# Kernel optimization log

Hardware: AMD Instinct MI355X
Metric: run time of the kernel (lower is better)

## Reference

```python
import jax, jax.numpy as jnp
import numpy as np

N, G, E, F, H = 100000, 32768, 1000000, 128, 128

def _mlp(x, w1, b1, w2, b2):
    # Linear -> SiLU -> Linear
    return jax.nn.silu(x @ w1 + b1) @ w2 + b2

def setup_inputs() -> dict:
    key = jax.random.key(0)
    ks = jax.random.split(key, 24)
    s = 0.02
    p = lambda k, shp: (jax.random.normal(k, shp, dtype=jnp.float32) * s)
    inp = {
        "node_features": jax.random.normal(ks[0], (N, F), dtype=jnp.float32),
        "node_pos": jax.random.normal(ks[1], (N, 3), dtype=jnp.float32),
        "grid_pos": jax.random.normal(ks[2], (G, 3), dtype=jnp.float32),
        "edge_index": jax.random.randint(ks[3], (2, E), 0, G, dtype=jnp.int64),
        "orientations": jax.random.normal(ks[4], (N, 3, 3), dtype=jnp.float32),
        # node_model
        "nw1": p(ks[5], (F, H)), "nb1": p(ks[6], (H,)),
        "nw2": p(ks[7], (H, H)), "nb2": p(ks[8], (H,)),
        # edge_model
        "ew1": p(ks[9], (6, H)), "eb1": p(ks[10], (H,)),
        "ew2": p(ks[11], (H, H)), "eb2": p(ks[12], (H,)),
        # message_model
        "mw1": p(ks[13], (2 * H, H)), "mb1": p(ks[14], (H,)),
        "mw2": p(ks[15], (H, H)), "mb2": p(ks[16], (H,)),
        # update_model
        "uw1": p(ks[17], (H, H)), "ub1": p(ks[18], (H,)),
        "uw2": p(ks[19], (H, H)), "ub2": p(ks[20], (H,)),
    }
    return inp

def reference(node_features, node_pos, grid_pos, edge_index, orientations,
              nw1, nb1, nw2, nb2, ew1, eb1, ew2, eb2,
              mw1, mb1, mw2, mb2, uw1, ub1, uw2, ub2):
    src, tgt = edge_index[0], edge_index[1]
    # node MLP on all points [N, H]
    node_h = _mlp(node_features, nw1, nb1, nw2, nb2)
    # per-edge geometry
    pos_src = node_pos[src]                     # [E, 3]
    rel_pos = grid_pos[tgt] - pos_src           # [E, 3]
    # bmm(rel_pos[e,1,3], orientations[src][e,3,3]) -> [E, 3]
    rot = jnp.einsum("ej,ejk->ek", rel_pos, orientations[src])
    edge_attr = jnp.concatenate([pos_src, rot], axis=-1)       # [E, 6]
    edge_h = _mlp(edge_attr, ew1, eb1, ew2, eb2)               # [E, H]
    msg_in = jnp.concatenate([node_h[src], edge_h], axis=-1)   # [E, 2H]
    msg = _mlp(msg_in, mw1, mb1, mw2, mb2)                     # [E, H]
    # scatter-mean to grid
    num_grid = grid_pos.shape[0]
    sums = jax.ops.segment_sum(msg, tgt, num_segments=num_grid)             # [G, H]
    counts = jax.ops.segment_sum(jnp.ones((msg.shape[0],), msg.dtype), tgt,
                                 num_segments=num_grid)
    grid_feat = sums / jnp.clip(counts, 1.0)[:, None]
    return _mlp(grid_feat, uw1, ub1, uw2, ub2)
```

## Files before the change

### kernel.cpp

```cpp
#include <hip/hip_runtime.h>

#define P 136

typedef __attribute__((ext_vector_type(8))) short short8;
typedef __attribute__((ext_vector_type(4))) float f32x4;

__device__ __forceinline__ unsigned short f2bf(float f) {
  union { float f; unsigned u; } v; v.f = f;
  unsigned u = v.u + 0x7fffu + ((v.u >> 16) & 1u);
  return (unsigned short)(u >> 16);
}
__device__ __forceinline__ float bf2f(unsigned short h) {
  union { unsigned u; float f; } v; v.u = ((unsigned)h) << 16;
  return v.f;
}
__device__ __forceinline__ unsigned pack2bf(float x, float y) {
  union { float f; unsigned u; } a, b; a.f = x; b.f = y;
  return __builtin_amdgcn_perm(b.u + 0x8000u, a.u + 0x8000u, 0x07060302u);
}
__device__ __forceinline__ float silu_f(float x) {
  float e = __expf(-x);
  return x * __builtin_amdgcn_rcpf(1.0f + e);
}

__device__ __forceinline__ void load_A128(const unsigned short* __restrict__ W,
                                          int m0w, int l16, int q, short8 a[2][4]) {
#pragma unroll
  for (int rt = 0; rt < 2; ++rt)
#pragma unroll
    for (int kt = 0; kt < 4; ++kt)
      a[rt][kt] = *(const short8*)&W[(m0w + rt * 16 + l16) * 128 + kt * 32 + q * 8];
}

template <int CT, bool INIT>
__device__ __forceinline__ void gemm_T(const short8 a[2][4],
                                       const unsigned short* sB,
                                       int l16, int q, f32x4 acc[2][CT]) {
  const f32x4 Z = (f32x4){0.f, 0.f, 0.f, 0.f};
#pragma unroll
  for (int kt = 0; kt < 4; ++kt)
#pragma unroll
    for (int ct = 0; ct < CT; ++ct) {
      short8 b = *(const short8*)&sB[(ct * 16 + l16) * P + kt * 32 + q * 8];
      f32x4 c0 = (INIT && kt == 0) ? Z : acc[0][ct];
      f32x4 c1 = (INIT && kt == 0) ? Z : acc[1][ct];
      acc[0][ct] = __builtin_amdgcn_mfma_f32_16x16x32_bf16(a[0][kt], b, c0, 0, 0, 0);
      acc[1][ct] = __builtin_amdgcn_mfma_f32_16x16x32_bf16(a[1][kt], b, c1, 0, 0, 0);
    }
}

template <bool SILU, int CT>
__device__ __forceinline__ void epilogue_T(const f32x4 acc[2][CT], const float* bias,
                                           unsigned short* sOut, int m0w, int l16,
                                           int q) {
#pragma unroll
  for (int rt = 0; rt < 2; ++rt) {
    int f0 = m0w + rt * 16 + q * 4;
    float4 bv = *(const float4*)&bias[f0];
#pragma unroll
    for (int ct = 0; ct < CT; ++ct) {
      float v0 = acc[rt][ct][0] + bv.x, v1 = acc[rt][ct][1] + bv.y;
      float v2 = acc[rt][ct][2] + bv.z, v3 = acc[rt][ct][3] + bv.w;
      if (SILU) { v0 = silu_f(v0); v1 = silu_f(v1); v2 = silu_f(v2); v3 = silu_f(v3); }
      uint2 w; w.x = pack2bf(v0, v1); w.y = pack2bf(v2, v3);
      *(uint2*)&sOut[(ct * 16 + l16) * P + f0] = w;
    }
  }
}

__global__ __launch_bounds__(256) void fold_hist_kernel(
    const float* __restrict__ nw1, const float* __restrict__ nw2,
    const float* __restrict__ nb2, const float* __restrict__ ew2,
    const float* __restrict__ eb2, const float* __restrict__ mw1,
    const float* __restrict__ mb1, const float* __restrict__ mw2,
    const float* __restrict__ uw1, const float* __restrict__ uw2,
    const float* __restrict__ ew1,
    unsigned short* __restrict__ nw1t, unsigned short* __restrict__ wnt,
    unsigned short* __restrict__ wct, unsigned short* __restrict__ mw2t,
    unsigned short* __restrict__ uw1t, unsigned short* __restrict__ uw2t,
    unsigned short* __restrict__ ew1t8,
    float* __restrict__ bn, float* __restrict__ bc,
    const int* __restrict__ eidx, int* __restrict__ hist, int E) {
  if (blockIdx.x >= 64) {
    int e0 = (blockIdx.x - 64) * 2048 + threadIdx.x * 8;
    if (e0 + 7 < E && (E & 3) == 0) {
      int4 t0 = *(const int4*)&eidx[E + e0];
      int4 t1 = *(const int4*)&eidx[E + e0 + 4];
      atomicAdd(&hist[t0.x], 1); atomicAdd(&hist[t0.y], 1);
      atomicAdd(&hist[t0.z], 1); atomicAdd(&hist[t0.w], 1);
      atomicAdd(&hist[t1.x], 1); atomicAdd(&hist[t1.y], 1);
      atomicAdd(&hist[t1.z], 1); atomicAdd(&hist[t1.w], 1);
    } else {
#pragma unroll
      for (int k = 0; k < 8; ++k) {
        int e = e0 + k;
        if (e < E) atomicAdd(&hist[eidx[E + e]], 1);
      }
    }
    return;
  }
  int b = blockIdx.x * 2 + (threadIdx.x >> 7);
  int t = threadIdx.x & 127;
  float accn = 0.f, accc = 0.f;
  for (int j = 0; j < 128; ++j) {
    accn += nw2[t * 128 + j] * mw1[j * 128 + b];
    accc += ew2[t * 128 + j] * mw1[(128 + j) * 128 + b];
  }
  wnt[b * 128 + t] = f2bf(accn);
  wct[b * 128 + t] = f2bf(accc);
  nw1t[b * 128 + t] = f2bf(nw1[t * 128 + b]);
  mw2t[b * 128 + t] = f2bf(mw2[t * 128 + b]);
  uw1t[b * 128 + t] = f2bf(uw1[t * 128 + b]);
  uw2t[b * 128 + t] = f2bf(uw2[t * 128 + b]);
  if (t < 8) ew1t8[b * 8 + t] = (t < 6) ? f2bf(ew1[t * 128 + b]) : (unsigned short)0;
  if (b == 0) {
    float sn = 0.f, sc = 0.f;
    for (int j = 0; j < 128; ++j) {
      sn += nb2[j] * mw1[j * 128 + t];
      sc += eb2[j] * mw1[(128 + j) * 128 + t];
    }
    bn[t] = sn;
    bc[t] = mb1[t] + sc;
  }
}

__global__ __launch_bounds__(1024) void scan_kernel(const int* __restrict__ hist,
                                                    int* __restrict__ cursor, int G) {
  __shared__ int s[1024];
  int tid = threadIdx.x;
  int per = (G + 1023) >> 10;
  int b0 = tid * per;
  bool vec = ((per & 3) == 0) && ((G & 3) == 0) && (b0 + per <= G);
  int sum = 0;
  if (vec) {
    for (int i = 0; i < per; i += 4) {
      int4 h = *(const int4*)&hist[b0 + i];
      sum += h.x + h.y + h.z + h.w;
    }
  } else {
    for (int i = 0; i < per; ++i)
      if (b0 + i < G) sum += hist[b0 + i];
  }
  s[tid] = sum;
  __syncthreads();
  for (int off = 1; off < 1024; off <<= 1) {
    int v = (tid >= off) ? s[tid - off] : 0;
    __syncthreads();
    s[tid] += v;
    __syncthreads();
  }
  int run = s[tid] - sum;
  if (vec) {
    for (int i = 0; i < per; i += 4) {
      int4 h = *(const int4*)&hist[b0 + i];
      int4 c;
      c.x = run;
      c.y = c.x + h.x;
      c.z = c.y + h.y;
      c.w = c.z + h.z;
      *(int4*)&cursor[b0 + i] = c;
      run = c.w + h.w;
    }
  } else {
    for (int i = 0; i < per; ++i)
      if (b0 + i < G) {
        cursor[b0 + i] = run;
        run += hist[b0 + i];
      }
  }
}

__global__ __launch_bounds__(256, 3) void scatter_node_kernel(
    const int* __restrict__ eidx, int* __restrict__ cursor,
    int2* __restrict__ st, int E, int nNode,
    const float* __restrict__ x, const float* __restrict__ nb1,
    const unsigned short* __restrict__ nw1t, const unsigned short* __restrict__ wnt,
    const float* __restrict__ bn, unsigned short* __restrict__ node_pre, int N) {
  __shared__ __align__(16) unsigned short s_x[128 * P];
  __shared__ __align__(16) float s_b1[128];
  __shared__ __align__(16) float s_bn[128];

  if (blockIdx.x >= (unsigned)nNode) {
    int e0 = (blockIdx.x - nNode) * 2048 + threadIdx.x * 8;
    if (e0 + 7 < E && (E & 3) == 0) {
      int4 s0 = *(const int4*)&eidx[e0];
      int4 s1 = *(const int4*)&eidx[e0 + 4];
      int4 t0 = *(const int4*)&eidx[E + e0];
      int4 t1 = *(const int4*)&eidx[E + e0 + 4];
      int p0 = atomicAdd(&cursor[t0.x], 1);
      int p1 = atomicAdd(&cursor[t0.y], 1);
      int p2 = atomicAdd(&cursor[t0.z], 1);
      int p3 = atomicAdd(&cursor[t0.w], 1);
      int p4 = atomicAdd(&cursor[t1.x], 1);
      int p5 = atomicAdd(&cursor[t1.y], 1);
      int p6 = atomicAdd(&cursor[t1.z], 1);
      int p7 = atomicAdd(&cursor[t1.w], 1);
      st[p0] = make_int2(s0.x, t0.x);
      st[p1] = make_int2(s0.y, t0.y);
      st[p2] = make_int2(s0.z, t0.z);
      st[p3] = make_int2(s0.w, t0.w);
      st[p4] = make_int2(s1.x, t1.x);
      st[p5] = make_int2(s1.y, t1.y);
      st[p6] = make_int2(s1.z, t1.z);
      st[p7] = make_int2(s1.w, t1.w);
    } else {
#pragma unroll
      for (int k = 0; k < 8; ++k) {
        int e = e0 + k;
        if (e < E) {
          int tg = eidx[E + e];
          int pos = atomicAdd(&cursor[tg], 1);
          st[pos] = make_int2(eidx[e], tg);
        }
      }
    }
    return;
  }

  int tid = threadIdx.x;
  long base = (long)blockIdx.x * 128;

#pragma unroll
  for (int i = 0; i < 16; ++i) {
    int flat = tid + i * 256;
    int row = flat >> 5;
    int c4 = (flat & 31) << 2;
    float4 v = make_float4(0.f, 0.f, 0.f, 0.f);
    if (base + row < N) v = *(const float4*)&x[(base + row) * 128 + c4];
    uint2 w; w.x = pack2bf(v.x, v.y); w.y = pack2bf(v.z, v.w);
    *(uint2*)&s_x[row * P + c4] = w;
  }
  if (tid < 128) { s_b1[tid] = nb1[tid]; s_bn[tid] = bn[tid]; }
  __syncthreads();

  int wave = tid >> 6, lane = tid & 63;
  int q = lane >> 4, l16 = lane & 15;
  int m0w = wave * 32;

  short8 a1[2][4];
  load_A128(nw1t, m0w, l16, q, a1);
  f32x4 acc[2][8];
  gemm_T<8, true>(a1, s_x, l16, q, acc);
  __syncthreads();
  epilogue_T<true, 8>(acc, s_b1, s_x, m0w, l16, q);
  __syncthreads();

  short8 a2[2][4];
  load_A128(wnt, m0w, l16, q, a2);
  gemm_T<8, true>(a2, s_x, l16, q, acc);

#pragma unroll
  for (int rt = 0; rt < 2; ++rt) {
    int f0 = m0w + rt * 16 + q * 4;
    float4 bv = *(const float4*)&s_bn[f0];
#pragma unroll
    for (int ct = 0; ct < 8; ++ct) {
      long n = base + ct * 16 + l16;
      if (n < N) {
        uint2 w;
        w.x = pack2bf(acc[rt][ct][0] + bv.x, acc[rt][ct][1] + bv.y);
        w.y = pack2bf(acc[rt][ct][2] + bv.z, acc[rt][ct][3] + bv.w);
        *(uint2*)&node_pre[n * 128 + f0] = w;
      }
    }
  }
}

__global__ __launch_bounds__(256, 3) void edge_kernel(
    const int2* __restrict__ st_sorted, const float* __restrict__ node_pos,
    const float* __restrict__ grid_pos, const float* __restrict__ ori,
    const unsigned short* __restrict__ ew1t8, const float* __restrict__ eb1,
    const unsigned short* __restrict__ wct, const float* __restrict__ bc,
    const unsigned short* __restrict__ node_pre, float* __restrict__ sums, int E) {
  __shared__ __align__(16) unsigned short s_h[128 * P];
  __shared__ int s_src[128];
  __shared__ int s_tgt[128];
  __shared__ __align__(16) float s_eb1[128];
  __shared__ __align__(16) float s_bc[128];

  int tid = threadIdx.x;
  int base = blockIdx.x * 128;

  if (tid < 128) {
    s_eb1[tid] = eb1[tid];
    s_bc[tid] = bc[tid];
    int eg = base + tid;
    int s = 0, tg = -1;
    float a0 = 0.f, a1 = 0.f, a2 = 0.f, a3 = 0.f, a4 = 0.f, a5 = 0.f;
    if (eg < E) {
      int2 st = st_sorted[eg];
      s = st.x; tg = st.y;
      float2 p01 = *(const float2*)&node_pos[s * 3];
      float pz = node_pos[s * 3 + 2];
      float2 g01 = *(const float2*)&grid_pos[tg * 3];
      float gz = grid_pos[tg * 3 + 2];
      float4 o0 = *(const float4*)&ori[(long)s * 9];
      float4 o1 = *(const float4*)&ori[(long)s * 9 + 4];
      float o8 = ori[(long)s * 9 + 8];
      float rx = g01.x - p01.x, ry = g01.y - p01.y, rz = gz - pz;
      a0 = p01.x; a1 = p01.y; a2 = pz;
      a3 = rx * o0.x + ry * o0.w + rz * o1.z;
      a4 = rx * o0.y + ry * o1.x + rz * o1.w;
      a5 = rx * o0.z + ry * o1.y + rz * o8;
    }
    s_src[tid] = s;
    s_tgt[tid] = tg;
    uint4 w0;
    w0.x = pack2bf(a0, a1); w0.y = pack2bf(a2, a3); w0.z = pack2bf(a4, a5); w0.w = 0u;
    *(uint4*)&s_h[tid * P] = w0;
  }

  int wave = tid >> 6, lane = tid & 63;
  int q = lane >> 4, l16 = lane & 15;
  int m0w = wave * 32;
  short8 z8 = (short8){0, 0, 0, 0, 0, 0, 0, 0};
  const f32x4 Z = (f32x4){0.f, 0.f, 0.f, 0.f};

  short8 ae0 = z8, ae1 = z8;
  if (q == 0) {
    ae0 = *(const short8*)&ew1t8[(m0w + l16) * 8];
    ae1 = *(const short8*)&ew1t8[(m0w + 16 + l16) * 8];
  }

  __syncthreads();

  short8 pre[8];
#pragma unroll
  for (int ct = 0; ct < 8; ++ct) {
    long srow = (long)s_src[ct * 16 + l16] * 128;
    pre[ct] = *(const short8*)&node_pre[srow + m0w + q * 8];
  }

  f32x4 acc[2][8];
#pragma unroll
  for (int ct = 0; ct < 8; ++ct) {
    short8 b = z8;
    if (q == 0) b = *(const short8*)&s_h[(ct * 16 + l16) * P];
    acc[0][ct] = __builtin_amdgcn_mfma_f32_16x16x32_bf16(ae0, b, Z, 0, 0, 0);
    acc[1][ct] = __builtin_amdgcn_mfma_f32_16x16x32_bf16(ae1, b, Z, 0, 0, 0);
  }
  __syncthreads();

  epilogue_T<true, 8>(acc, s_eb1, s_h, m0w, l16, q);

  short8 awc[2][4];
  load_A128(wct, m0w, l16, q, awc);

  __syncthreads();

  short8 aI_lo, aI_hi;
#pragma unroll
  for (int j = 0; j < 8; ++j) {
    aI_lo[j] = ((q * 8 + j) == l16) ? (short)0x3F80 : (short)0;
    aI_hi[j] = ((q * 8 + j) == (l16 + 16)) ? (short)0x3F80 : (short)0;
  }
#pragma unroll
  for (int ct = 0; ct < 8; ++ct) {
    acc[0][ct] = __builtin_amdgcn_mfma_f32_16x16x32_bf16(aI_lo, pre[ct], Z, 0, 0, 0);
    acc[1][ct] = __builtin_amdgcn_mfma_f32_16x16x32_bf16(aI_hi, pre[ct], Z, 0, 0, 0);
  }

  gemm_T<8, false>(awc, s_h, l16, q, acc);
  __syncthreads();

  epilogue_T<true, 8>(acc, s_bc, s_h, m0w, l16, q);
  __syncthreads();

  {
    int cp = tid & 63;
    int chunk = tid >> 6;
    int c0 = cp * 2;
    int row0 = chunk * 32;
    float v0 = 0.f, v1 = 0.f;
    int cur = s_tgt[row0];
    for (int r = 0; r < 32; ++r) {
      int row = row0 + r;
      int tg = s_tgt[row];
      if (tg != cur) {
        if (cur >= 0) {
          atomicAdd(&sums[(long)cur * 128 + c0], v0);
          atomicAdd(&sums[(long)cur * 128 + c0 + 1], v1);
        }
        v0 = 0.f; v1 = 0.f; cur = tg;
      }
      unsigned w = *(const unsigned*)&s_h[row * P + c0];
      v0 += bf2f((unsigned short)w);
      v1 += bf2f((unsigned short)(w >> 16));
    }
    if (cur >= 0) {
      atomicAdd(&sums[(long)cur * 128 + c0], v0);
      atomicAdd(&sums[(long)cur * 128 + c0 + 1], v1);
    }
  }
}

__global__ __launch_bounds__(256, 3) void grid_kernel(
    const float* __restrict__ sums, const int* __restrict__ hist,
    const float* __restrict__ mb2, const float* __restrict__ ub1,
    const float* __restrict__ ub2, const unsigned short* __restrict__ mw2t,
    const unsigned short* __restrict__ uw1t, const unsigned short* __restrict__ uw2t,
    float* __restrict__ out, int G) {
  __shared__ __align__(16) unsigned short s_x[32 * P];
  __shared__ __align__(16) float s_bm[128];
  __shared__ __align__(16) float s_b1[128];
  __shared__ __align__(16) float s_b2[128];
  int tid = threadIdx.x;
  long base = (long)blockIdx.x * 32;

#pragma unroll
  for (int i = 0; i < 4; ++i) {
    int flat = tid + i * 256;
    int row = flat >> 5;
    int c4 = (flat & 31) << 2;
    float4 v = make_float4(0.f, 0.f, 0.f, 0.f);
    float inv = 1.f;
    if (base + row < G) {
      v = *(const float4*)&sums[(base + row) * 128 + c4];
      int c = hist[base + row];
      inv = __builtin_amdgcn_rcpf((float)(c < 1 ? 1 : c));
    }
    uint2 w; w.x = pack2bf(v.x * inv, v.y * inv); w.y = pack2bf(v.z * inv, v.w * inv);
    *(uint2*)&s_x[row * P + c4] = w;
  }
  if (tid < 128) { s_bm[tid] = mb2[tid]; s_b1[tid] = ub1[tid]; s_b2[tid] = ub2[tid]; }
  __syncthreads();

  int wave = tid >> 6, lane = tid & 63;
  int q = lane >> 4, l16 = lane & 15;
  int m0w = wave * 32;

  f32x4 acc[2][2];
  short8 aw[2][4];

  load_A128(mw2t, m0w, l16, q, aw);
  gemm_T<2, true>(aw, s_x, l16, q, acc);
  __syncthreads();
  epilogue_T<false, 2>(acc, s_bm, s_x, m0w, l16, q);
  __syncthreads();

  load_A128(uw1t, m0w, l16, q, aw);
  gemm_T<2, true>(aw, s_x, l16, q, acc);
  __syncthreads();
  epilogue_T<true, 2>(acc, s_b1, s_x, m0w, l16, q);
  __syncthreads();

  load_A128(uw2t, m0w, l16, q, aw);
  gemm_T<2, true>(aw, s_x, l16, q, acc);

#pragma unroll
  for (int rt = 0; rt < 2; ++rt) {
    int f0 = m0w + rt * 16 + q * 4;
    float4 bv = *(const float4*)&s_b2[f0];
#pragma unroll
    for (int ct = 0; ct < 2; ++ct) {
      long g = base + ct * 16 + l16;
      if (g < G) {
        float4 o = make_float4(acc[rt][ct][0] + bv.x, acc[rt][ct][1] + bv.y,
                               acc[rt][ct][2] + bv.z, acc[rt][ct][3] + bv.w);
        *(float4*)&out[g * 128 + f0] = o;
      }
    }
  }
}

extern "C" void kernel_launch(void* const* d_in, const int* in_sizes, int n_in,
                              void* d_out, int out_size, void* d_ws, size_t ws_size,
                              hipStream_t stream) {
  const float* x    = (const float*)d_in[0];
  const float* npos = (const float*)d_in[1];
  const float* gpos = (const float*)d_in[2];
  const int*   eidx = (const int*)d_in[3];
  const float* ori  = (const float*)d_in[4];
  const float* nw1 = (const float*)d_in[5];
  const float* nb1 = (const float*)d_in[6];
  const float* nw2 = (const float*)d_in[7];
  const float* nb2 = (const float*)d_in[8];
  const float* ew1 = (const float*)d_in[9];
  const float* eb1 = (const float*)d_in[10];
  const float* ew2 = (const float*)d_in[11];
  const float* eb2 = (const float*)d_in[12];
  const float* mw1 = (const float*)d_in[13];
  const float* mb1 = (const float*)d_in[14];
  const float* mw2 = (const float*)d_in[15];
  const float* mb2 = (const float*)d_in[16];
  const float* uw1 = (const float*)d_in[17];
  const float* ub1 = (const float*)d_in[18];
  const float* uw2 = (const float*)d_in[19];
  const float* ub2 = (const float*)d_in[20];

  int N = in_sizes[0] / 128;
  int G = in_sizes[2] / 3;
  int E = in_sizes[3] / 2;

  char* ws = (char*)d_ws;
  size_t off = 0;
  float* sums = (float*)(ws + off);            off += (size_t)G * 128 * 4;
  int* hist = (int*)(ws + off);                off += (size_t)G * 4;
  int* cursor = (int*)(ws + off);              off += (size_t)G * 4;
  unsigned short* node_pre = (unsigned short*)(ws + off); off += (size_t)N * 128 * 2;
  off = (off + 255) & ~(size_t)255;
  unsigned short* w_nw1t = (unsigned short*)(ws + off); off += 128 * 128 * 2;
  unsigned short* w_wnt  = (unsigned short*)(ws + off); off += 128 * 128 * 2;
  unsigned short* w_wct  = (unsigned short*)(ws + off); off += 128 * 128 * 2;
  unsigned short* w_mw2t = (unsigned short*)(ws + off); off += 128 * 128 * 2;
  unsigned short* w_uw1t = (unsigned short*)(ws + off); off += 128 * 128 * 2;
  unsigned short* w_uw2t = (unsigned short*)(ws + off); off += 128 * 128 * 2;
  unsigned short* w_ew1t8 = (unsigned short*)(ws + off); off += 128 * 8 * 2;
  float* bn = (float*)(ws + off); off += 128 * 4;
  float* bc = (float*)(ws + off); off += 128 * 4;

  int2* st_sorted = (int2*)d_out;

  int nScat = (E + 2047) / 2048;
  int nNode = (N + 127) / 128;
  int nHist = (E + 2047) / 2048;

  hipMemsetAsync(sums, 0, ((size_t)G * 128 + G) * 4, stream);

  fold_hist_kernel<<<64 + nHist, 256, 0, stream>>>(
      nw1, nw2, nb2, ew2, eb2, mw1, mb1, mw2, uw1, uw2, ew1,
      w_nw1t, w_wnt, w_wct, w_mw2t, w_uw1t, w_uw2t, w_ew1t8, bn, bc,
      eidx, hist, E);
  scan_kernel<<<1, 1024, 0, stream>>>(hist, cursor, G);
  scatter_node_kernel<<<nNode + nScat, 256, 0, stream>>>(
      eidx, cursor, st_sorted, E, nNode,
      x, nb1, w_nw1t, w_wnt, bn, node_pre, N);
  edge_kernel<<<(E + 127) / 128, 256, 0, stream>>>(st_sorted, npos, gpos, ori,
                                                   w_ew1t8, eb1, w_wct, bc,
                                                   node_pre, sums, E);
  grid_kernel<<<(G + 31) / 32, 256, 0, stream>>>(sums, hist, mb2, ub1, ub2,
                                                 w_mw2t, w_uw1t, w_uw2t,
                                                 (float*)d_out, G);
}
```

Before: 395.9 us.

## Double edges per thread in hist/scatter, raise edge occupancy, widen segment reduce

The histogram and scatter blocks now handle 16 edges per thread instead of 8, which halves their block counts and issues more independent loads and atomics per thread. The edge kernel's launch bounds ask for 4 blocks per CU instead of 3, which may force register spills. The final segment reduction gives each thread 4 columns over 16 rows instead of 2 columns over 32 rows, so runs are cut into shorter chunks and more global atomics may be issued per target.

```diff
diff --git a/kernel.cpp b/kernel.cpp
--- a/kernel.cpp
+++ b/kernel.cpp
@@ -82,17 +82,23 @@
     float* __restrict__ bn, float* __restrict__ bc,
     const int* __restrict__ eidx, int* __restrict__ hist, int E) {
   if (blockIdx.x >= 64) {
-    int e0 = (blockIdx.x - 64) * 2048 + threadIdx.x * 8;
-    if (e0 + 7 < E && (E & 3) == 0) {
+    int e0 = (blockIdx.x - 64) * 4096 + threadIdx.x * 16;
+    if (e0 + 15 < E && (E & 3) == 0) {
       int4 t0 = *(const int4*)&eidx[E + e0];
       int4 t1 = *(const int4*)&eidx[E + e0 + 4];
+      int4 t2 = *(const int4*)&eidx[E + e0 + 8];
+      int4 t3 = *(const int4*)&eidx[E + e0 + 12];
       atomicAdd(&hist[t0.x], 1); atomicAdd(&hist[t0.y], 1);
       atomicAdd(&hist[t0.z], 1); atomicAdd(&hist[t0.w], 1);
       atomicAdd(&hist[t1.x], 1); atomicAdd(&hist[t1.y], 1);
       atomicAdd(&hist[t1.z], 1); atomicAdd(&hist[t1.w], 1);
+      atomicAdd(&hist[t2.x], 1); atomicAdd(&hist[t2.y], 1);
+      atomicAdd(&hist[t2.z], 1); atomicAdd(&hist[t2.w], 1);
+      atomicAdd(&hist[t3.x], 1); atomicAdd(&hist[t3.y], 1);
+      atomicAdd(&hist[t3.z], 1); atomicAdd(&hist[t3.w], 1);
     } else {
 #pragma unroll
-      for (int k = 0; k < 8; ++k) {
+      for (int k = 0; k < 16; ++k) {
         int e = e0 + k;
         if (e < E) atomicAdd(&hist[eidx[E + e]], 1);
       }
@@ -181,36 +187,37 @@
   __shared__ __align__(16) float s_bn[128];
 
   if (blockIdx.x >= (unsigned)nNode) {
-    int e0 = (blockIdx.x - nNode) * 2048 + threadIdx.x * 8;
-    if (e0 + 7 < E && (E & 3) == 0) {
-      int4 s0 = *(const int4*)&eidx[e0];
-      int4 s1 = *(const int4*)&eidx[e0 + 4];
-      int4 t0 = *(const int4*)&eidx[E + e0];
-      int4 t1 = *(const int4*)&eidx[E + e0 + 4];
-      int p0 = atomicAdd(&cursor[t0.x], 1);
-      int p1 = atomicAdd(&cursor[t0.y], 1);
-      int p2 = atomicAdd(&cursor[t0.z], 1);
-      int p3 = atomicAdd(&cursor[t0.w], 1);
-      int p4 = atomicAdd(&cursor[t1.x], 1);
-      int p5 = atomicAdd(&cursor[t1.y], 1);
-      int p6 = atomicAdd(&cursor[t1.z], 1);
-      int p7 = atomicAdd(&cursor[t1.w], 1);
-      st[p0] = make_int2(s0.x, t0.x);
-      st[p1] = make_int2(s0.y, t0.y);
-      st[p2] = make_int2(s0.z, t0.z);
-      st[p3] = make_int2(s0.w, t0.w);
-      st[p4] = make_int2(s1.x, t1.x);
-      st[p5] = make_int2(s1.y, t1.y);
-      st[p6] = make_int2(s1.z, t1.z);
-      st[p7] = make_int2(s1.w, t1.w);
+    int e0 = (blockIdx.x - nNode) * 4096 + threadIdx.x * 16;
+    if (e0 + 15 < E && (E & 3) == 0) {
+      int4 sv[4], tv[4];
+#pragma unroll
+      for (int g = 0; g < 4; ++g) {
+        sv[g] = *(const int4*)&eidx[e0 + g * 4];
+        tv[g] = *(const int4*)&eidx[E + e0 + g * 4];
+      }
+      int pos[16];
+#pragma unroll
+      for (int g = 0; g < 4; ++g) {
+        pos[g * 4 + 0] = atomicAdd(&cursor[tv[g].x], 1);
+        pos[g * 4 + 1] = atomicAdd(&cursor[tv[g].y], 1);
+        pos[g * 4 + 2] = atomicAdd(&cursor[tv[g].z], 1);
+        pos[g * 4 + 3] = atomicAdd(&cursor[tv[g].w], 1);
+      }
+#pragma unroll
+      for (int g = 0; g < 4; ++g) {
+        st[pos[g * 4 + 0]] = make_int2(sv[g].x, tv[g].x);
+        st[pos[g * 4 + 1]] = make_int2(sv[g].y, tv[g].y);
+        st[pos[g * 4 + 2]] = make_int2(sv[g].z, tv[g].z);
+        st[pos[g * 4 + 3]] = make_int2(sv[g].w, tv[g].w);
+      }
     } else {
 #pragma unroll
-      for (int k = 0; k < 8; ++k) {
+      for (int k = 0; k < 16; ++k) {
         int e = e0 + k;
         if (e < E) {
           int tg = eidx[E + e];
-          int pos = atomicAdd(&cursor[tg], 1);
-          st[pos] = make_int2(eidx[e], tg);
+          int p = atomicAdd(&cursor[tg], 1);
+          st[p] = make_int2(eidx[e], tg);
         }
       }
     }
@@ -266,7 +273,7 @@
   }
 }
 
-__global__ __launch_bounds__(256, 3) void edge_kernel(
+__global__ __launch_bounds__(256, 4) void edge_kernel(
     const int2* __restrict__ st_sorted, const float* __restrict__ node_pos,
     const float* __restrict__ grid_pos, const float* __restrict__ ori,
     const unsigned short* __restrict__ ew1t8, const float* __restrict__ eb1,
@@ -367,29 +374,35 @@
   __syncthreads();
 
   {
-    int cp = tid & 63;
-    int chunk = tid >> 6;
-    int c0 = cp * 2;
-    int row0 = chunk * 32;
-    float v0 = 0.f, v1 = 0.f;
+    int cq = tid & 31;
+    int chunk = tid >> 5;
+    int c0 = cq * 4;
+    int row0 = chunk * 16;
+    float v0 = 0.f, v1 = 0.f, v2 = 0.f, v3 = 0.f;
     int cur = s_tgt[row0];
-    for (int r = 0; r < 32; ++r) {
+    for (int r = 0; r < 16; ++r) {
       int row = row0 + r;
       int tg = s_tgt[row];
       if (tg != cur) {
         if (cur >= 0) {
           atomicAdd(&sums[(long)cur * 128 + c0], v0);
           atomicAdd(&sums[(long)cur * 128 + c0 + 1], v1);
+          atomicAdd(&sums[(long)cur * 128 + c0 + 2], v2);
+          atomicAdd(&sums[(long)cur * 128 + c0 + 3], v3);
         }
-        v0 = 0.f; v1 = 0.f; cur = tg;
-      }
-      unsigned w = *(const unsigned*)&s_h[row * P + c0];
-      v0 += bf2f((unsigned short)w);
-      v1 += bf2f((unsigned short)(w >> 16));
+        v0 = 0.f; v1 = 0.f; v2 = 0.f; v3 = 0.f; cur = tg;
+      }
+      uint2 w = *(const uint2*)&s_h[row * P + c0];
+      v0 += bf2f((unsigned short)w.x);
+      v1 += bf2f((unsigned short)(w.x >> 16));
+      v2 += bf2f((unsigned short)w.y);
+      v3 += bf2f((unsigned short)(w.y >> 16));
     }
     if (cur >= 0) {
       atomicAdd(&sums[(long)cur * 128 + c0], v0);
       atomicAdd(&sums[(long)cur * 128 + c0 + 1], v1);
+      atomicAdd(&sums[(long)cur * 128 + c0 + 2], v2);
+      atomicAdd(&sums[(long)cur * 128 + c0 + 3], v3);
     }
   }
 }
@@ -511,9 +524,9 @@
 
   int2* st_sorted = (int2*)d_out;
 
-  int nScat = (E + 2047) / 2048;
+  int nScat = (E + 4095) / 4096;
   int nNode = (N + 127) / 128;
-  int nHist = (E + 2047) / 2048;
+  int nHist = (E + 4095) / 4096;
 
   hipMemsetAsync(sums, 0, ((size_t)G * 128 + G) * 4, stream);
 
```

Measured after the change: 465.4 us. 1.18x slower.
